# Optimization experiments

Measured on AMD Instinct MI355X. Metric: run time of the kernel, lower is better.

Reference implementation:

```python
import jax, jax.numpy as jnp
import numpy as np

HIDDEN_DIM = 1000
CONTEXT_DIM = 2000


def setup_inputs() -> dict:
    key = jax.random.key(0)
    k1, k2, k3, k4 = jax.random.split(key, 4)
    B, N = 64, 1024
    std = 0.001
    return {
        "s_prev": jax.random.normal(k1, (B, HIDDEN_DIM), dtype=jnp.float32),
        "h_j": jax.random.normal(k2, (B, N, CONTEXT_DIM), dtype=jnp.float32),
        "W_a": jax.random.normal(k3, (HIDDEN_DIM, HIDDEN_DIM), dtype=jnp.float32) * std,
        "U_a": jax.random.normal(k4, (HIDDEN_DIM, CONTEXT_DIM), dtype=jnp.float32) * std,
        "v_a": jnp.zeros((HIDDEN_DIM,), dtype=jnp.float32),
    }


def reference(s_prev, h_j, W_a, U_a, v_a):
    # W_a s: (B, H); U_a h: (B, N, H)
    W_a_s = jnp.einsum("bd,hd->bh", s_prev, W_a)
    U_a_h = jnp.einsum("bnc,hc->bnh", h_j, U_a)
    energy = jnp.tanh(W_a_s[:, None, :] + U_a_h)  # (B, N, H)
    scores = jnp.einsum("bnh,h->bn", energy, v_a)  # (B, N)
    return scores
```

## Files before the change

kernel.cpp:

```cpp
#include <hip/hip_runtime.h>
#include <hip/hip_bf16.h>

#define HID 1000
#define CTX 2000
#define KP   2016
#define HP   1024
#define BATCH 64
#define NSEQ 1024
#define M_TOT (BATCH * NSEQ)
#define WSTR 1024

typedef __attribute__((ext_vector_type(8))) short short8;
typedef __attribute__((ext_vector_type(4))) float floatx4;

__device__ __forceinline__ unsigned short f2bf(float x) {
    union { float f; unsigned u; } v; v.f = x;
    unsigned r = v.u + 0x7FFFu + ((v.u >> 16) & 1u);
    return (unsigned short)(r >> 16);
}

typedef const __attribute__((address_space(1))) unsigned glb_u32;
typedef __attribute__((address_space(3))) unsigned lds_u32;
__device__ __forceinline__ void gload16(const void* g, void* l) {
    __builtin_amdgcn_global_load_lds((glb_u32*)g, (lds_u32*)l, 16, 0, 0);
}

__global__ void zero_kernel(float* __restrict__ out, int n) {
    int i = blockIdx.x * 256 + threadIdx.x;
    if (i < n) out[i] = 0.0f;
}

__global__ void convertA_kernel(const float* __restrict__ src, unsigned short* __restrict__ dst) {
    int row = blockIdx.x;
    int t = threadIdx.x;
    if (t >= KP / 8) return;
    unsigned short pk[8];
    if (t < CTX / 8) {
        const float* p = src + (size_t)row * CTX + t * 8;
        float4 a = *(const float4*)p;
        float4 b = *(const float4*)(p + 4);
        pk[0]=f2bf(a.x); pk[1]=f2bf(a.y); pk[2]=f2bf(a.z); pk[3]=f2bf(a.w);
        pk[4]=f2bf(b.x); pk[5]=f2bf(b.y); pk[6]=f2bf(b.z); pk[7]=f2bf(b.w);
    } else {
#pragma unroll
        for (int i = 0; i < 8; i++) pk[i] = 0;
    }
    *(short8*)(dst + (size_t)row * KP + t * 8) = *(short8*)pk;
}

__global__ void convertB_kernel(const float* __restrict__ src, unsigned short* __restrict__ dst) {
    int row = blockIdx.x;
    int t = threadIdx.x;
    if (t >= KP / 8) return;
    unsigned short pk[8];
    if (row < HID && t < CTX / 8) {
        const float* p = src + (size_t)row * CTX + t * 8;
        float4 a = *(const float4*)p;
        float4 b = *(const float4*)(p + 4);
        pk[0]=f2bf(a.x); pk[1]=f2bf(a.y); pk[2]=f2bf(a.z); pk[3]=f2bf(a.w);
        pk[4]=f2bf(b.x); pk[5]=f2bf(b.y); pk[6]=f2bf(b.z); pk[7]=f2bf(b.w);
    } else {
#pragma unroll
        for (int i = 0; i < 8; i++) pk[i] = 0;
    }
    *(short8*)(dst + (size_t)row * KP + t * 8) = *(short8*)pk;
}

__global__ void ws_kernel(const float* __restrict__ s_prev,
                          const float* __restrict__ W_a,
                          float* __restrict__ W_s) {
    int wave = threadIdx.x >> 6, lane = threadIdx.x & 63;
    int gw = blockIdx.x * 4 + wave;
    int b = gw / HID, h = gw % HID;
    const float* wr = W_a + (size_t)h * HID;
    const float* sr = s_prev + (size_t)b * HID;
    float acc = 0.0f;
#pragma unroll
    for (int it = 0; it < 4; ++it) {
        int idx = it * 64 + lane;
        if (idx < HID / 4) {
            float4 w = *(const float4*)(wr + idx * 4);
            float4 s = *(const float4*)(sr + idx * 4);
            acc += w.x * s.x + w.y * s.y + w.z * s.z + w.w * s.w;
        }
    }
    acc += __shfl_xor(acc, 1);
    acc += __shfl_xor(acc, 2);
    acc += __shfl_xor(acc, 4);
    acc += __shfl_xor(acc, 8);
    acc += __shfl_xor(acc, 16);
    acc += __shfl_xor(acc, 32);
    if (lane == 0) W_s[b * WSTR + h] = acc;
}

__global__ __launch_bounds__(256, 2) void gemm_kernel(
        const unsigned short* __restrict__ A, const unsigned short* __restrict__ B,
        const float* __restrict__ W_s, const float* __restrict__ v_a,
        float* __restrict__ out) {
    __shared__ __align__(16) unsigned short As[128 * 32];
    __shared__ __align__(16) unsigned short Bs[128 * 32];

    const int tid  = threadIdx.x;
    const int lane = tid & 63;
    const int wave = tid >> 6;
    const int wm = wave & 1, wh = wave >> 1;
    const int ln = lane & 15, quad = lane >> 4;

    const int m0 = blockIdx.x * 128;
    const int b  = m0 >> 10;

    const int srow = lane >> 2;
    const int scol = (lane & 3) * 8;
    const unsigned short* abase0 = A + (size_t)(m0 + wave * 16 + srow) * KP + scol;
    const unsigned short* abase1 = abase0 + (size_t)64 * KP;
    unsigned short* asl0 = &As[(wave * 16) * 32];
    unsigned short* asl1 = &As[(64 + wave * 16) * 32];
    unsigned short* bsl0 = &Bs[(wave * 16) * 32];
    unsigned short* bsl1 = &Bs[(64 + wave * 16) * 32];

    float rowsum[4][4];
#pragma unroll
    for (int i = 0; i < 4; i++)
#pragma unroll
        for (int r = 0; r < 4; r++) rowsum[i][r] = 0.0f;

    for (int ht = 0; ht < HP / 128; ++ht) {
        const unsigned short* aptr0 = abase0;
        const unsigned short* aptr1 = abase1;
        const unsigned short* bptr0 = B + (size_t)(ht * 128 + wave * 16 + srow) * KP + scol;
        const unsigned short* bptr1 = bptr0 + (size_t)64 * KP;

        floatx4 acc[4][4];
#pragma unroll
        for (int i = 0; i < 4; i++)
#pragma unroll
            for (int j = 0; j < 4; j++) acc[i][j] = (floatx4)0.0f;

        for (int kk = 0; kk < KP / 32; ++kk) {
            __syncthreads();
            gload16(aptr0, asl0);
            gload16(aptr1, asl1);
            gload16(bptr0, bsl0);
            gload16(bptr1, bsl1);
            aptr0 += 32; aptr1 += 32; bptr0 += 32; bptr1 += 32;
            __syncthreads();

            short8 af[4], bfr[4];
#pragma unroll
            for (int i = 0; i < 4; i++)
                af[i] = *(const short8*)&As[(wm * 64 + i * 16 + ln) * 32 + quad * 8];
#pragma unroll
            for (int j = 0; j < 4; j++)
                bfr[j] = *(const short8*)&Bs[(wh * 64 + j * 16 + ln) * 32 + quad * 8];
#pragma unroll
            for (int i = 0; i < 4; i++)
#pragma unroll
                for (int j = 0; j < 4; j++)
                    acc[i][j] = __builtin_amdgcn_mfma_f32_16x16x32_bf16(af[i], bfr[j], acc[i][j], 0, 0, 0);
        }

#pragma unroll
        for (int j = 0; j < 4; j++) {
            const int h = ht * 128 + wh * 64 + j * 16 + ln;
            float wsv = 0.0f, vav = 0.0f;
            if (h < HID) { wsv = W_s[b * WSTR + h]; vav = v_a[h]; }
#pragma unroll
            for (int i = 0; i < 4; i++)
#pragma unroll
                for (int r = 0; r < 4; r++)
                    rowsum[i][r] += vav * tanhf(acc[i][j][r] + wsv);
        }
    }

#pragma unroll
    for (int i = 0; i < 4; i++)
#pragma unroll
        for (int r = 0; r < 4; r++) {
            float v = rowsum[i][r];
            v += __shfl_xor(v, 1);
            v += __shfl_xor(v, 2);
            v += __shfl_xor(v, 4);
            v += __shfl_xor(v, 8);
            rowsum[i][r] = v;
        }

    if (ln == 0) {
#pragma unroll
        for (int i = 0; i < 4; i++) {
            const int row = m0 + wm * 64 + i * 16 + quad * 4;
#pragma unroll
            for (int r = 0; r < 4; r++)
                atomicAdd(&out[row + r], rowsum[i][r]);
        }
    }
}

extern "C" void kernel_launch(void* const* d_in, const int* in_sizes, int n_in,
                              void* d_out, int out_size, void* d_ws, size_t ws_size,
                              hipStream_t stream) {
    const float* s_prev = (const float*)d_in[0];
    const float* h_j    = (const float*)d_in[1];
    const float* W_a    = (const float*)d_in[2];
    const float* U_a    = (const float*)d_in[3];
    const float* v_a    = (const float*)d_in[4];
    float* out = (float*)d_out;

    const size_t b_off = 64 * WSTR * sizeof(float);
    const size_t a_off = b_off + (size_t)HP * KP * sizeof(short);
    float* W_s = (float*)d_ws;
    unsigned short* B_bf = (unsigned short*)((char*)d_ws + b_off);
    unsigned short* A_bf = (unsigned short*)((char*)d_ws + a_off);

    zero_kernel<<<dim3(M_TOT / 256), 256, 0, stream>>>(out, M_TOT);
    ws_kernel<<<dim3(BATCH * HID / 4), 256, 0, stream>>>(s_prev, W_a, W_s);
    convertA_kernel<<<dim3(M_TOT), 256, 0, stream>>>(h_j, A_bf);
    convertB_kernel<<<dim3(HP), 256, 0, stream>>>(U_a, B_bf);
    gemm_kernel<<<dim3(M_TOT / 128), 256, 0, stream>>>(A_bf, B_bf, W_s, v_a, out);
}
```

Baseline: 1.195 ms.

## Fuse fp32-to-bf16 conversion of h_j into GEMM with double-buffered LDS and XCD-aware grid

Drops the separate convertA pass: the GEMM now reads h_j in fp32 straight into registers, converts it with v_cvt_pk_bf16_f32 and writes bf16 into LDS. The main loop is double-buffered so the next K tile is prefetched while MFMAs run on the current one, with one barrier per step. The H tiles now go to separate blocks, remapped so blocks sharing an A row tile land on the same XCD, and occupancy is raised to 3 blocks per CU. This removes the write and re-read of a large bf16 copy of h_j, but each of the 8 H-tile blocks now reads the fp32 A tile again, doubling A bytes per read, which the shared L2 should absorb.

```diff
diff --git a/kernel.cpp b/kernel.cpp
--- a/kernel.cpp
+++ b/kernel.cpp
@@ -19,6 +19,12 @@
     return (unsigned short)(r >> 16);
 }
 
+__device__ __forceinline__ unsigned pkbf(float lo, float hi) {
+    unsigned r;
+    asm("v_cvt_pk_bf16_f32 %0, %1, %2" : "=v"(r) : "v"(lo), "v"(hi));
+    return r;
+}
+
 typedef const __attribute__((address_space(1))) unsigned glb_u32;
 typedef __attribute__((address_space(3))) unsigned lds_u32;
 __device__ __forceinline__ void gload16(const void* g, void* l) {
@@ -28,24 +34,6 @@
 __global__ void zero_kernel(float* __restrict__ out, int n) {
     int i = blockIdx.x * 256 + threadIdx.x;
     if (i < n) out[i] = 0.0f;
-}
-
-__global__ void convertA_kernel(const float* __restrict__ src, unsigned short* __restrict__ dst) {
-    int row = blockIdx.x;
-    int t = threadIdx.x;
-    if (t >= KP / 8) return;
-    unsigned short pk[8];
-    if (t < CTX / 8) {
-        const float* p = src + (size_t)row * CTX + t * 8;
-        float4 a = *(const float4*)p;
-        float4 b = *(const float4*)(p + 4);
-        pk[0]=f2bf(a.x); pk[1]=f2bf(a.y); pk[2]=f2bf(a.z); pk[3]=f2bf(a.w);
-        pk[4]=f2bf(b.x); pk[5]=f2bf(b.y); pk[6]=f2bf(b.z); pk[7]=f2bf(b.w);
-    } else {
-#pragma unroll
-        for (int i = 0; i < 8; i++) pk[i] = 0;
-    }
-    *(short8*)(dst + (size_t)row * KP + t * 8) = *(short8*)pk;
 }
 
 __global__ void convertB_kernel(const float* __restrict__ src, unsigned short* __restrict__ dst) {
@@ -93,12 +81,13 @@
     if (lane == 0) W_s[b * WSTR + h] = acc;
 }
 
-__global__ __launch_bounds__(256, 2) void gemm_kernel(
-        const unsigned short* __restrict__ A, const unsigned short* __restrict__ B,
+__global__ __launch_bounds__(256, 3) void gemm_kernel(
+        const float* __restrict__ A,
+        const unsigned short* __restrict__ B,
         const float* __restrict__ W_s, const float* __restrict__ v_a,
         float* __restrict__ out) {
-    __shared__ __align__(16) unsigned short As[128 * 32];
-    __shared__ __align__(16) unsigned short Bs[128 * 32];
+    __shared__ __align__(16) unsigned short As[2 * 128 * 32];
+    __shared__ __align__(16) unsigned short Bs[2 * 128 * 32];
 
     const int tid  = threadIdx.x;
     const int lane = tid & 63;
@@ -106,17 +95,92 @@
     const int wm = wave & 1, wh = wave >> 1;
     const int ln = lane & 15, quad = lane >> 4;
 
-    const int m0 = blockIdx.x * 128;
-    const int b  = m0 >> 10;
-
-    const int srow = lane >> 2;
-    const int scol = (lane & 3) * 8;
-    const unsigned short* abase0 = A + (size_t)(m0 + wave * 16 + srow) * KP + scol;
-    const unsigned short* abase1 = abase0 + (size_t)64 * KP;
-    unsigned short* asl0 = &As[(wave * 16) * 32];
-    unsigned short* asl1 = &As[(64 + wave * 16) * 32];
-    unsigned short* bsl0 = &Bs[(wave * 16) * 32];
-    unsigned short* bsl1 = &Bs[(64 + wave * 16) * 32];
+    const int bid = blockIdx.x;
+    const int xcd = bid & 7, seq = bid >> 3;
+    const int m0 = (xcd * 64 + (seq >> 3)) * 128;
+    const int ht = seq & 7;
+    const int bb = m0 >> 10;
+
+    const int arow = tid >> 1, ahalf = tid & 1;
+    const float* abase = A + (size_t)(m0 + arow) * CTX + ahalf * 16;
+    const int aoff = arow * 64 + ahalf * 32;
+
+    const int srow = lane >> 2, scol = (lane & 3) * 8;
+    const unsigned short* bbase0 = B + (size_t)(ht * 128 + wave * 16 + srow) * KP + scol;
+    const unsigned short* bbase1 = bbase0 + (size_t)64 * KP;
+    const int bw0 = (wave * 16) * 32;
+    const int bw1 = (64 + wave * 16) * 32;
+
+    floatx4 acc[4][4];
+#pragma unroll
+    for (int i = 0; i < 4; i++)
+#pragma unroll
+        for (int j = 0; j < 4; j++) acc[i][j] = (floatx4)0.0f;
+
+    float4 ra0, ra1, ra2, ra3;
+
+    ra0 = *(const float4*)(abase);
+    ra1 = *(const float4*)(abase + 4);
+    ra2 = *(const float4*)(abase + 8);
+    ra3 = *(const float4*)(abase + 12);
+    gload16(bbase0, Bs + bw0);
+    gload16(bbase1, Bs + bw1);
+    {
+        unsigned w0 = pkbf(ra0.x, ra0.y), w1 = pkbf(ra0.z, ra0.w);
+        unsigned w2 = pkbf(ra1.x, ra1.y), w3 = pkbf(ra1.z, ra1.w);
+        unsigned w4 = pkbf(ra2.x, ra2.y), w5 = pkbf(ra2.z, ra2.w);
+        unsigned w6 = pkbf(ra3.x, ra3.y), w7 = pkbf(ra3.z, ra3.w);
+        *(uint4*)((char*)As + aoff)      = make_uint4(w0, w1, w2, w3);
+        *(uint4*)((char*)As + aoff + 16) = make_uint4(w4, w5, w6, w7);
+    }
+    __syncthreads();
+
+    int p = 0;
+    for (int kk = 0; kk < 63; ++kk) {
+        unsigned short* an = As + ((p ^ 1) << 12);
+        unsigned short* bn = Bs + ((p ^ 1) << 12);
+        const unsigned short* ap_ = As + (p << 12);
+        const unsigned short* bp_ = Bs + (p << 12);
+
+        const bool pre = (kk < 62);
+        if (pre) {
+            const float* gp = abase + (size_t)(kk + 1) * 32;
+            if ((kk + 1) * 32 + ahalf * 16 < CTX) {
+                ra0 = *(const float4*)(gp);
+                ra1 = *(const float4*)(gp + 4);
+                ra2 = *(const float4*)(gp + 8);
+                ra3 = *(const float4*)(gp + 12);
+            } else {
+                ra0 = ra1 = ra2 = ra3 = make_float4(0.f, 0.f, 0.f, 0.f);
+            }
+            gload16(bbase0 + (kk + 1) * 32, bn + bw0);
+            gload16(bbase1 + (kk + 1) * 32, bn + bw1);
+        }
+
+        short8 af[4], bfr[4];
+#pragma unroll
+        for (int i = 0; i < 4; i++)
+            af[i] = *(const short8*)&ap_[(wm * 64 + i * 16 + ln) * 32 + quad * 8];
+#pragma unroll
+        for (int j = 0; j < 4; j++)
+            bfr[j] = *(const short8*)&bp_[(wh * 64 + j * 16 + ln) * 32 + quad * 8];
+#pragma unroll
+        for (int i = 0; i < 4; i++)
+#pragma unroll
+            for (int j = 0; j < 4; j++)
+                acc[i][j] = __builtin_amdgcn_mfma_f32_16x16x32_bf16(af[i], bfr[j], acc[i][j], 0, 0, 0);
+
+        if (pre) {
+            unsigned w0 = pkbf(ra0.x, ra0.y), w1 = pkbf(ra0.z, ra0.w);
+            unsigned w2 = pkbf(ra1.x, ra1.y), w3 = pkbf(ra1.z, ra1.w);
+            unsigned w4 = pkbf(ra2.x, ra2.y), w5 = pkbf(ra2.z, ra2.w);
+            unsigned w6 = pkbf(ra3.x, ra3.y), w7 = pkbf(ra3.z, ra3.w);
+            *(uint4*)((char*)an + aoff)      = make_uint4(w0, w1, w2, w3);
+            *(uint4*)((char*)an + aoff + 16) = make_uint4(w4, w5, w6, w7);
+        }
+        __syncthreads();
+        p ^= 1;
+    }
 
     float rowsum[4][4];
 #pragma unroll
@@ -124,52 +188,16 @@
 #pragma unroll
         for (int r = 0; r < 4; r++) rowsum[i][r] = 0.0f;
 
-    for (int ht = 0; ht < HP / 128; ++ht) {
-        const unsigned short* aptr0 = abase0;
-        const unsigned short* aptr1 = abase1;
-        const unsigned short* bptr0 = B + (size_t)(ht * 128 + wave * 16 + srow) * KP + scol;
-        const unsigned short* bptr1 = bptr0 + (size_t)64 * KP;
-
-        floatx4 acc[4][4];
+#pragma unroll
+    for (int j = 0; j < 4; j++) {
+        const int h = ht * 128 + wh * 64 + j * 16 + ln;
+        float wsv = 0.0f, vav = 0.0f;
+        if (h < HID) { wsv = W_s[bb * WSTR + h]; vav = v_a[h]; }
 #pragma unroll
         for (int i = 0; i < 4; i++)
 #pragma unroll
-            for (int j = 0; j < 4; j++) acc[i][j] = (floatx4)0.0f;
-
-        for (int kk = 0; kk < KP / 32; ++kk) {
-            __syncthreads();
-            gload16(aptr0, asl0);
-            gload16(aptr1, asl1);
-            gload16(bptr0, bsl0);
-            gload16(bptr1, bsl1);
-            aptr0 += 32; aptr1 += 32; bptr0 += 32; bptr1 += 32;
-            __syncthreads();
-
-            short8 af[4], bfr[4];
-#pragma unroll
-            for (int i = 0; i < 4; i++)
-                af[i] = *(const short8*)&As[(wm * 64 + i * 16 + ln) * 32 + quad * 8];
-#pragma unroll
-            for (int j = 0; j < 4; j++)
-                bfr[j] = *(const short8*)&Bs[(wh * 64 + j * 16 + ln) * 32 + quad * 8];
-#pragma unroll
-            for (int i = 0; i < 4; i++)
-#pragma unroll
-                for (int j = 0; j < 4; j++)
-                    acc[i][j] = __builtin_amdgcn_mfma_f32_16x16x32_bf16(af[i], bfr[j], acc[i][j], 0, 0, 0);
-        }
-
-#pragma unroll
-        for (int j = 0; j < 4; j++) {
-            const int h = ht * 128 + wh * 64 + j * 16 + ln;
-            float wsv = 0.0f, vav = 0.0f;
-            if (h < HID) { wsv = W_s[b * WSTR + h]; vav = v_a[h]; }
-#pragma unroll
-            for (int i = 0; i < 4; i++)
-#pragma unroll
-                for (int r = 0; r < 4; r++)
-                    rowsum[i][r] += vav * tanhf(acc[i][j][r] + wsv);
-        }
+            for (int r = 0; r < 4; r++)
+                rowsum[i][r] += vav * tanhf(acc[i][j][r] + wsv);
     }
 
 #pragma unroll
@@ -206,14 +234,11 @@
     float* out = (float*)d_out;
 
     const size_t b_off = 64 * WSTR * sizeof(float);
-    const size_t a_off = b_off + (size_t)HP * KP * sizeof(short);
     float* W_s = (float*)d_ws;
     unsigned short* B_bf = (unsigned short*)((char*)d_ws + b_off);
-    unsigned short* A_bf = (unsigned short*)((char*)d_ws + a_off);
 
     zero_kernel<<<dim3(M_TOT / 256), 256, 0, stream>>>(out, M_TOT);
     ws_kernel<<<dim3(BATCH * HID / 4), 256, 0, stream>>>(s_prev, W_a, W_s);
-    convertA_kernel<<<dim3(M_TOT), 256, 0, stream>>>(h_j, A_bf);
     convertB_kernel<<<dim3(HP), 256, 0, stream>>>(U_a, B_bf);
-    gemm_kernel<<<dim3(M_TOT / 128), 256, 0, stream>>>(A_bf, B_bf, W_s, v_a, out);
-}
+    gemm_kernel<<<dim3((M_TOT / 128) * (HP / 128)), 256, 0, stream>>>(h_j, B_bf, W_s, v_a, out);
+}
```

After: 1.209 ms. No clear change (+1.1%).
